# Kernel optimization log

Measured on AMD Instinct MI355X. Metric: run time of the kernel, lower is better.

The kernel has to match this reference:

```python
import jax, jax.numpy as jnp
import numpy as np
from jax import lax

DIM = 2048
N_HEADS = 16
N_KV = 4
HEAD_DIM = DIM // N_HEADS  # 128
ROPE_BASE = 10000.0
SEQ = 4096
BSZ = 1


def bitlinear(x, W):
    # per-row abs-mean scale (detached), ternary round/clamp, straight-through blend
    s = lax.stop_gradient(jnp.clip(jnp.mean(jnp.abs(W), axis=1, keepdims=True), 1e-5, None))
    wt = jnp.clip(jnp.round(W / s), -1.0, 1.0)
    w = lax.stop_gradient(wt - W) + W  # straight-through
    return x @ (w * s).T


def rms_norm(x):
    eps = jnp.finfo(x.dtype).eps
    return x * lax.rsqrt(jnp.mean(x * x, axis=-1, keepdims=True) + eps)


def rope(x, cos, sin):
    half = x.shape[-1] // 2
    x1, x2 = x[..., :half], x[..., half:]
    return jnp.concatenate((x1 * cos + x2 * sin, -x1 * sin + x2 * cos), axis=-1)


def setup_inputs() -> dict:
    key = jax.random.key(0)
    ks = jax.random.split(key, 6)
    kv_dim = N_KV * HEAD_DIM
    return {
        "x": jax.random.normal(ks[0], (BSZ, SEQ, DIM), dtype=jnp.float32),
        "wq": jax.random.normal(ks[1], (DIM, DIM), dtype=jnp.float32) * 0.02,
        "wk": jax.random.normal(ks[2], (kv_dim, DIM), dtype=jnp.float32) * 0.02,
        "wv": jax.random.normal(ks[3], (kv_dim, DIM), dtype=jnp.float32) * 0.02,
        "wp": jax.random.normal(ks[4], (DIM, DIM), dtype=jnp.float32) * 0.02,
        "q_gain": jnp.ones((N_HEADS,), dtype=jnp.float32),
    }


def reference(x, wq, wk, wv, wp, q_gain):
    b, s, d = x.shape
    q = bitlinear(x, wq).reshape(b, s, N_HEADS, HEAD_DIM).transpose(0, 2, 1, 3)  # bhsd
    k = bitlinear(x, wk).reshape(b, s, N_KV, HEAD_DIM).transpose(0, 2, 1, 3)
    v = bitlinear(x, wv).reshape(b, s, N_KV, HEAD_DIM).transpose(0, 2, 1, 3)

    q = rms_norm(q)
    k = rms_norm(k)

    inv_freq = 1.0 / ROPE_BASE ** (jnp.arange(0, HEAD_DIM, 2, dtype=jnp.float32) / HEAD_DIM)
    t = jnp.arange(s, dtype=jnp.float32)
    freqs = jnp.outer(t, inv_freq)  # [s, hd/2]
    cos = jnp.cos(freqs)[None, None].astype(q.dtype)
    sin = jnp.sin(freqs)[None, None].astype(q.dtype)
    q = rope(q, cos, sin)
    k = rope(k, cos, sin)

    q = q * q_gain.astype(q.dtype)[None, :, None, None]

    groups = N_HEADS // N_KV
    k = jnp.repeat(k, groups, axis=1)  # GQA expand to [b, H, s, hd]
    v = jnp.repeat(v, groups, axis=1)

    scale = 1.0 / np.sqrt(HEAD_DIM)
    scores = jnp.einsum("bhqd,bhkd->bhqk", q, k) * scale
    causal = jnp.tril(jnp.ones((s, s), dtype=bool))
    scores = jnp.where(causal[None, None], scores, jnp.finfo(scores.dtype).min)
    attn = jax.nn.softmax(scores, axis=-1)
    y = jnp.einsum("bhqk,bhkd->bhqd", attn, v)

    y = y.transpose(0, 2, 1, 3).reshape(b, s, d)
    return bitlinear(y, wp)
```

## Files before the change

### kernel.cpp

```cpp
#include <hip/hip_runtime.h>
#include <math.h>

typedef unsigned short u16;
typedef short s16x8 __attribute__((ext_vector_type(8)));
typedef short s16x4 __attribute__((ext_vector_type(4)));
typedef float f32x4 __attribute__((ext_vector_type(4)));
typedef u16 u16x4 __attribute__((ext_vector_type(4)));

static constexpr size_t OFF_XB   = 0;
static constexpr size_t OFF_WQKV = 16777216;
static constexpr size_t OFF_WP   = 29360128;
static constexpr size_t OFF_QKV  = 37748736;
static constexpr size_t OFF_Y    = 37748736 + 33554432;
static constexpr size_t OFF_KH   = 88080384;
static constexpr size_t OFF_VT   = 92274688;

__device__ __forceinline__ u16 f2bf(float f) {
  union { float f; unsigned u; } v; v.f = f;
  unsigned r = v.u + 0x7fffu + ((v.u >> 16) & 1u);
  return (u16)(r >> 16);
}

__device__ __forceinline__ float bf2f(u16 b) {
  union { unsigned u; float f; } v; v.u = ((unsigned)b) << 16;
  return v.f;
}

__device__ __forceinline__ void async16(const u16* g, u16* lds) {
  __builtin_amdgcn_global_load_lds(
      (const __attribute__((address_space(1))) void*)g,
      (__attribute__((address_space(3))) void*)lds, 16, 0, 0);
}

__global__ __launch_bounds__(256) void quant_rows(const float* __restrict__ W,
                                                  u16* __restrict__ out) {
  const int row = blockIdx.x, tid = threadIdx.x;
  const float* src = W + (size_t)row * 2048 + tid * 8;
  float4 a = *(const float4*)(src);
  float4 b = *(const float4*)(src + 4);
  float asum = fabsf(a.x)+fabsf(a.y)+fabsf(a.z)+fabsf(a.w)
             + fabsf(b.x)+fabsf(b.y)+fabsf(b.z)+fabsf(b.w);
  #pragma unroll
  for (int off = 1; off < 64; off <<= 1) asum += __shfl_xor(asum, off, 64);
  __shared__ float red[4];
  if ((tid & 63) == 0) red[tid >> 6] = asum;
  __syncthreads();
  float s = fmaxf((red[0]+red[1]+red[2]+red[3]) * (1.0f/2048.0f), 1e-5f);
  float v[8] = {a.x,a.y,a.z,a.w,b.x,b.y,b.z,b.w};
  u16* dst = out + (size_t)row * 2048 + tid * 8;
  #pragma unroll
  for (int i = 0; i < 8; i++) {
    float q = rintf(v[i] / s);
    q = fminf(fmaxf(q, -1.f), 1.f);
    dst[i] = f2bf(q * s);
  }
}

__global__ __launch_bounds__(256) void cvt_bf16(const float* __restrict__ in,
                                                u16* __restrict__ out) {
  size_t i = ((size_t)blockIdx.x * 256 + threadIdx.x) * 4;
  float4 v = *(const float4*)(in + i);
  u16x4 o;
  o.x = f2bf(v.x); o.y = f2bf(v.y); o.z = f2bf(v.z); o.w = f2bf(v.w);
  *(u16x4*)(out + i) = o;
}

__global__ __launch_bounds__(256) void gemm_bt(const u16* __restrict__ A,
                                               const u16* __restrict__ B,
                                               float* __restrict__ C,
                                               int M, int N, int K) {
  __shared__ u16 sA[128 * 32];
  __shared__ u16 sB[128 * 32];
  const int tid = threadIdx.x;
  const int lane = tid & 63;
  const int wid = tid >> 6;
  const int lr = lane & 15, lq = lane >> 4;
  const int wm = (wid >> 1) * 64, wn = (wid & 1) * 64;
  const size_t m0 = (size_t)blockIdx.y * 128, n0 = (size_t)blockIdx.x * 128;

  const int r0 = tid >> 2, c0 = (tid & 3) * 8;
  const u16* Ab0 = A + (m0 + r0) * (size_t)K + c0;
  const u16* Ab1 = A + (m0 + 64 + r0) * (size_t)K + c0;
  const u16* Bb0 = B + (n0 + r0) * (size_t)K + c0;
  const u16* Bb1 = B + (n0 + 64 + r0) * (size_t)K + c0;
  u16* sA0 = &sA[tid * 8];
  u16* sA1 = &sA[(256 + tid) * 8];
  u16* sB0 = &sB[tid * 8];
  u16* sB1 = &sB[(256 + tid) * 8];

  f32x4 acc[4][4] = {};

  for (int kt = 0; kt < K; kt += 32) {
    async16(Ab0 + kt, sA0);
    async16(Ab1 + kt, sA1);
    async16(Bb0 + kt, sB0);
    async16(Bb1 + kt, sB1);
    __syncthreads();
    s16x8 af[4], bf[4];
    #pragma unroll
    for (int mt = 0; mt < 4; mt++)
      af[mt] = *(const s16x8*)&sA[(wm + mt * 16 + lr) * 32 + lq * 8];
    #pragma unroll
    for (int nt = 0; nt < 4; nt++)
      bf[nt] = *(const s16x8*)&sB[(wn + nt * 16 + lr) * 32 + lq * 8];
    #pragma unroll
    for (int mt = 0; mt < 4; mt++)
      #pragma unroll
      for (int nt = 0; nt < 4; nt++)
        acc[mt][nt] = __builtin_amdgcn_mfma_f32_16x16x32_bf16(af[mt], bf[nt], acc[mt][nt], 0, 0, 0);
    __syncthreads();
  }
  #pragma unroll
  for (int mt = 0; mt < 4; mt++)
    #pragma unroll
    for (int nt = 0; nt < 4; nt++)
      #pragma unroll
      for (int r = 0; r < 4; r++) {
        size_t m = m0 + wm + mt * 16 + lq * 4 + r;
        size_t n = n0 + wn + nt * 16 + lr;
        C[m * (size_t)N + n] = acc[mt][nt][r];
      }
}

__global__ __launch_bounds__(256) void prep_qk(const float* __restrict__ qkv,
                                               const float* __restrict__ qgain,
                                               u16* __restrict__ Qh,
                                               u16* __restrict__ Kh) {
  const int s = blockIdx.y;
  const int j = blockIdx.x * 4 + (threadIdx.x >> 6);
  const int t = threadIdx.x & 63;
  const float* row = qkv + (size_t)s * 3072 + (size_t)j * 128;
  float x1 = row[t], x2 = row[t + 64];
  float ss = x1 * x1 + x2 * x2;
  #pragma unroll
  for (int off = 1; off < 64; off <<= 1) ss += __shfl_xor(ss, off, 64);
  float rn = rsqrtf(ss * (1.0f / 128.0f) + 1.1920929e-07f);
  float invf = exp2f(-(float)t * 0.20762050593048096f);
  float ang = (float)s * invf;
  float sn, c;
  sincosf(ang, &sn, &c);
  if (j < 16) {
    float g = qgain[j] * 0.12751738f;
    float q1 = x1 * rn, q2 = x2 * rn;
    float o1 = (q1 * c + q2 * sn) * g;
    float o2 = (-q1 * sn + q2 * c) * g;
    u16* dst = Qh + ((size_t)j * 4096 + s) * 128;
    dst[t] = f2bf(o1); dst[t + 64] = f2bf(o2);
  } else {
    float k1 = x1 * rn, k2 = x2 * rn;
    float o1 = k1 * c + k2 * sn;
    float o2 = -k1 * sn + k2 * c;
    u16* dst = Kh + ((size_t)(j - 16) * 4096 + s) * 128;
    dst[t] = f2bf(o1); dst[t + 64] = f2bf(o2);
  }
}

__global__ __launch_bounds__(256) void vtrans(const float* __restrict__ qkv,
                                              u16* __restrict__ Vtg) {
  __shared__ float tile[64][67];
  const int tid = threadIdx.x;
  const int s0 = blockIdx.y * 64;
  const int c0 = blockIdx.x * 64;
  #pragma unroll
  for (int it = 0; it < 4; it++) {
    int i = it * 256 + tid;
    int r = i >> 4, c = (i & 15) * 4;
    float4 v = *(const float4*)(qkv + (size_t)(s0 + r) * 3072 + 2560 + c0 + c);
    tile[r][c] = v.x; tile[r][c + 1] = v.y; tile[r][c + 2] = v.z; tile[r][c + 3] = v.w;
  }
  __syncthreads();
  #pragma unroll
  for (int it = 0; it < 2; it++) {
    int i = it * 256 + tid;
    int dl = i >> 3, sc = (i & 7) * 8;
    s16x8 ov;
    #pragma unroll
    for (int jj = 0; jj < 8; jj++) ov[jj] = (short)f2bf(tile[sc + jj][dl]);
    *(s16x8*)&Vtg[(size_t)(c0 + dl) * 4096 + s0 + sc] = ov;
  }
}

__global__ __launch_bounds__(256, 2) void attn(const u16* __restrict__ Q,
                                               const u16* __restrict__ Kh,
                                               const u16* __restrict__ Vt,
                                               u16* __restrict__ Opart,
                                               float* __restrict__ MLpart) {
  const int tid = threadIdx.x, lane = tid & 63, wid = tid >> 6;
  const int lr = lane & 15, lq = lane >> 4;

  const int b = blockIdx.x;
  const int h = b & 15;
  const int p = b >> 4;
  const int qt = 31 - (p >> 1);
  const int chunk = p & 1;
  const int t0 = chunk * (qt + 1);
  const int t1 = t0 + qt + 1;
  const int kvh = h >> 2;
  const int qbase = qt * 128;

  __shared__ u16 sK[64][136];
  __shared__ u16 sVt[128][72];

  s16x8 qf[2][4];
  #pragma unroll
  for (int f = 0; f < 2; f++) {
    const u16* qp = Q + ((size_t)h * 4096 + qbase + wid * 32 + f * 16 + lr) * 128 + lq * 8;
    #pragma unroll
    for (int kc = 0; kc < 4; kc++) qf[f][kc] = *(const s16x8*)(qp + kc * 32);
  }

  f32x4 oacc[2][8] = {};
  float mrow[2] = {-1e30f, -1e30f};
  float lrow[2] = {0.f, 0.f};

  const u16* Kbase = Kh + (size_t)kvh * 4096 * 128;
  const u16* Vbase = Vt + (size_t)kvh * 128 * 4096;

  for (int t = t0; t < t1; ++t) {
    #pragma unroll
    for (int it = 0; it < 4; it++) {
      int idx = it * 256 + tid;
      int kr = idx >> 4, kc8 = (idx & 15) * 8;
      *(s16x8*)&sK[kr][kc8] = *(const s16x8*)(Kbase + (size_t)(t * 64 + kr) * 128 + kc8);
    }
    #pragma unroll
    for (int it = 0; it < 4; it++) {
      int idx = it * 256 + tid;
      int vd = idx >> 3, vc = (idx & 7) * 8;
      s16x8 v = *(const s16x8*)(Vbase + (size_t)vd * 4096 + t * 64 + vc);
      int g0 = ((vc >> 2) & 3) * 16 + (vc >> 4) * 4;
      int g1 = (((vc >> 2) & 3) + 1) * 16 + (vc >> 4) * 4;
      s16x4 lo = {v[0], v[1], v[2], v[3]};
      s16x4 hi = {v[4], v[5], v[6], v[7]};
      *(s16x4*)&sVt[vd][g0] = lo;
      *(s16x4*)&sVt[vd][g1] = hi;
    }
    __syncthreads();

    f32x4 sacc[2][4] = {};
    #pragma unroll
    for (int nt = 0; nt < 4; nt++)
      #pragma unroll
      for (int kc = 0; kc < 4; kc++) {
        s16x8 kf = *(const s16x8*)&sK[nt * 16 + lr][kc * 32 + lq * 8];
        sacc[0][nt] = __builtin_amdgcn_mfma_f32_16x16x32_bf16(kf, qf[0][kc], sacc[0][nt], 0, 0, 0);
        sacc[1][nt] = __builtin_amdgcn_mfma_f32_16x16x32_bf16(kf, qf[1][kc], sacc[1][nt], 0, 0, 0);
      }

    if (t >= 2 * qt) {
      #pragma unroll
      for (int f = 0; f < 2; f++) {
        int qg = qbase + wid * 32 + f * 16 + lr;
        #pragma unroll
        for (int nt = 0; nt < 4; nt++) {
          int kv0 = t * 64 + nt * 16 + lq * 4;
          #pragma unroll
          for (int r = 0; r < 4; r++)
            if (kv0 + r > qg) sacc[f][nt][r] = -1e30f;
        }
      }
    }

    float mx[2];
    #pragma unroll
    for (int f = 0; f < 2; f++) {
      float m01 = fmaxf(fmaxf(sacc[f][0][0], sacc[f][0][1]), fmaxf(sacc[f][0][2], sacc[f][0][3]));
      float m23 = fmaxf(fmaxf(sacc[f][1][0], sacc[f][1][1]), fmaxf(sacc[f][1][2], sacc[f][1][3]));
      float m45 = fmaxf(fmaxf(sacc[f][2][0], sacc[f][2][1]), fmaxf(sacc[f][2][2], sacc[f][2][3]));
      float m67 = fmaxf(fmaxf(sacc[f][3][0], sacc[f][3][1]), fmaxf(sacc[f][3][2], sacc[f][3][3]));
      mx[f] = fmaxf(fmaxf(m01, m23), fmaxf(m45, m67));
      mx[f] = fmaxf(mx[f], __shfl_xor(mx[f], 16, 64));
      mx[f] = fmaxf(mx[f], __shfl_xor(mx[f], 32, 64));
    }

    bool grow = (mx[0] > mrow[0]) || (mx[1] > mrow[1]);
    if (__any(grow)) {
      #pragma unroll
      for (int f = 0; f < 2; f++) {
        float mn = fmaxf(mrow[f], mx[f]);
        float al = exp2f(mrow[f] - mn);
        mrow[f] = mn;
        lrow[f] *= al;
        #pragma unroll
        for (int dt = 0; dt < 8; dt++)
          #pragma unroll
          for (int r = 0; r < 4; r++) oacc[f][dt][r] *= al;
      }
    }

    s16x4 pf[2][4];
    float rsum[2] = {0.f, 0.f};
    #pragma unroll
    for (int f = 0; f < 2; f++)
      #pragma unroll
      for (int nt = 0; nt < 4; nt++)
        #pragma unroll
        for (int r = 0; r < 4; r++) {
          union { float fv; unsigned u; } pu;
          pu.fv = exp2f(sacc[f][nt][r] - mrow[f]);
          rsum[f] += pu.fv;
          pf[f][nt][r] = (short)(pu.u >> 16);
        }
    #pragma unroll
    for (int f = 0; f < 2; f++) {
      rsum[f] += __shfl_xor(rsum[f], 16, 64);
      rsum[f] += __shfl_xor(rsum[f], 32, 64);
      lrow[f] += rsum[f];
    }

    #pragma unroll
    for (int dt = 0; dt < 8; dt++) {
      s16x8 v01 = *(const s16x8*)&sVt[dt * 16 + lr][lq * 16];
      s16x8 v23 = *(const s16x8*)&sVt[dt * 16 + lr][lq * 16 + 8];
      s16x4 vf0 = {v01[0], v01[1], v01[2], v01[3]};
      s16x4 vf1 = {v01[4], v01[5], v01[6], v01[7]};
      s16x4 vf2 = {v23[0], v23[1], v23[2], v23[3]};
      s16x4 vf3 = {v23[4], v23[5], v23[6], v23[7]};
      #pragma unroll
      for (int f = 0; f < 2; f++) {
        oacc[f][dt] = __builtin_amdgcn_mfma_f32_16x16x16bf16_1k(vf0, pf[f][0], oacc[f][dt], 0, 0, 0);
        oacc[f][dt] = __builtin_amdgcn_mfma_f32_16x16x16bf16_1k(vf1, pf[f][1], oacc[f][dt], 0, 0, 0);
        oacc[f][dt] = __builtin_amdgcn_mfma_f32_16x16x16bf16_1k(vf2, pf[f][2], oacc[f][dt], 0, 0, 0);
        oacc[f][dt] = __builtin_amdgcn_mfma_f32_16x16x16bf16_1k(vf3, pf[f][3], oacc[f][dt], 0, 0, 0);
      }
    }
    __syncthreads();
  }

  u16* Op = Opart + (size_t)b * 16384;
  #pragma unroll
  for (int f = 0; f < 2; f++) {
    int row = wid * 32 + f * 16 + lr;
    #pragma unroll
    for (int dt = 0; dt < 8; dt++) {
      u16 tmp[4];
      #pragma unroll
      for (int r = 0; r < 4; r++) tmp[r] = f2bf(oacc[f][dt][r]);
      *(s16x4*)&Op[row * 128 + dt * 16 + lq * 4] = *(s16x4*)tmp;
    }
  }
  if (lq == 0) {
    #pragma unroll
    for (int f = 0; f < 2; f++) {
      int row = wid * 32 + f * 16 + lr;
      MLpart[(size_t)b * 256 + row * 2]     = mrow[f];
      MLpart[(size_t)b * 256 + row * 2 + 1] = lrow[f];
    }
  }
}

__global__ __launch_bounds__(256) void combine(const u16* __restrict__ Op,
                                               const float* __restrict__ ML,
                                               u16* __restrict__ Y) {
  const int blk = blockIdx.x;
  const int qtc = blk >> 4, h = blk & 15;
  const int qt = 31 - qtc;
  const int b0 = (qtc * 2) * 16 + h, b1 = b0 + 16;
  const int tid = threadIdx.x;
  const int row = tid >> 1, half = (tid & 1) * 64;
  float m0 = ML[(size_t)b0 * 256 + row * 2], l0 = ML[(size_t)b0 * 256 + row * 2 + 1];
  float m1 = ML[(size_t)b1 * 256 + row * 2], l1 = ML[(size_t)b1 * 256 + row * 2 + 1];
  float m = fmaxf(m0, m1);
  float w0 = exp2f(m0 - m), w1 = exp2f(m1 - m);
  float inv = 1.0f / (l0 * w0 + l1 * w1);
  w0 *= inv; w1 *= inv;
  const u16* o0 = Op + (size_t)b0 * 16384 + row * 128 + half;
  const u16* o1 = Op + (size_t)b1 * 16384 + row * 128 + half;
  size_t q = (size_t)qt * 128 + row;
  u16* dst = Y + q * 2048 + h * 128 + half;
  #pragma unroll
  for (int c = 0; c < 64; c += 8) {
    s16x8 a0 = *(const s16x8*)(o0 + c);
    s16x8 a1 = *(const s16x8*)(o1 + c);
    u16 tmp[8];
    #pragma unroll
    for (int jj = 0; jj < 8; jj++)
      tmp[jj] = f2bf(bf2f((u16)a0[jj]) * w0 + bf2f((u16)a1[jj]) * w1);
    *(s16x8*)(dst + c) = *(s16x8*)tmp;
  }
}

extern "C" void kernel_launch(void* const* d_in, const int* in_sizes, int n_in,
                              void* d_out, int out_size, void* d_ws, size_t ws_size,
                              hipStream_t stream) {
  const float* x  = (const float*)d_in[0];
  const float* wq = (const float*)d_in[1];
  const float* wk = (const float*)d_in[2];
  const float* wv = (const float*)d_in[3];
  const float* wp = (const float*)d_in[4];
  const float* qg = (const float*)d_in[5];
  float* out = (float*)d_out;
  char* ws = (char*)d_ws;

  u16*   XB    = (u16*)(ws + OFF_XB);
  u16*   WQKV  = (u16*)(ws + OFF_WQKV);
  u16*   WP    = (u16*)(ws + OFF_WP);
  float* QKV   = (float*)(ws + OFF_QKV);
  u16*   QH    = XB;
  u16*   KH    = (u16*)(ws + OFF_KH);
  u16*   VT    = (u16*)(ws + OFF_VT);
  u16*   OPART = (u16*)(ws + OFF_QKV);
  u16*   Yb    = (u16*)(ws + OFF_Y);
  float* MLP   = (float*)(ws + OFF_WQKV);

  quant_rows<<<2048, 256, 0, stream>>>(wq, WQKV);
  quant_rows<<<512,  256, 0, stream>>>(wk, WQKV + (size_t)2048 * 2048);
  quant_rows<<<512,  256, 0, stream>>>(wv, WQKV + (size_t)2560 * 2048);
  quant_rows<<<2048, 256, 0, stream>>>(wp, WP);
  cvt_bf16<<<8192, 256, 0, stream>>>(x, XB);
  gemm_bt<<<dim3(24, 32), 256, 0, stream>>>(XB, WQKV, QKV, 4096, 3072, 2048);
  prep_qk<<<dim3(5, 4096), 256, 0, stream>>>(QKV, qg, QH, KH);
  vtrans<<<dim3(8, 64), 256, 0, stream>>>(QKV, VT);
  attn<<<1024, 256, 0, stream>>>(QH, KH, VT, OPART, MLP);
  combine<<<512, 256, 0, stream>>>(OPART, MLP, Yb);
  gemm_bt<<<dim3(16, 32), 256, 0, stream>>>(Yb, WP, out, 4096, 2048, 2048);
}
```

Measured before the change: 419.9 us.

## Balance causal attention work with a precomputed segment table and direct writes

New measurement: 418.1 us. Within noise of the previous version (-0.4%).

```diff
diff --git a/kernel.cpp b/kernel.cpp
--- a/kernel.cpp
+++ b/kernel.cpp
@@ -9,11 +9,12 @@
 
 static constexpr size_t OFF_XB   = 0;
 static constexpr size_t OFF_WQKV = 16777216;
+static constexpr size_t OFF_KH   = 16777216;
+static constexpr size_t OFF_VT   = 20971520;
+static constexpr size_t OFF_ML   = 25165824;
 static constexpr size_t OFF_WP   = 29360128;
 static constexpr size_t OFF_QKV  = 37748736;
-static constexpr size_t OFF_Y    = 37748736 + 33554432;
-static constexpr size_t OFF_KH   = 88080384;
-static constexpr size_t OFF_VT   = 92274688;
+static constexpr size_t OFF_Y    = 79691776;
 
 __device__ __forceinline__ u16 f2bf(float f) {
   union { float f; unsigned u; } v; v.f = f;
@@ -180,171 +181,258 @@
   }
 }
 
+#define SEG(qt,a,b,s) ((unsigned)((qt)|((a)<<5)|((b)<<11)|((s)<<18)))
+__constant__ unsigned SEGTAB[128] = {
+  SEG(0,0,2,127),   SEG(15,0,15,14),
+  SEG(15,15,32,15), 0,
+  SEG(1,0,4,127),   SEG(14,0,13,12),
+  SEG(14,13,30,13), 0,
+  SEG(2,0,6,127),   SEG(13,0,11,10),
+  SEG(13,11,28,11), 0,
+  SEG(3,0,8,127),   SEG(12,0,9,8),
+  SEG(12,9,26,9),   0,
+  SEG(4,0,10,127),  SEG(11,0,7,6),
+  SEG(11,7,24,7),   0,
+  SEG(5,0,12,127),  SEG(10,0,5,4),
+  SEG(10,5,22,5),   0,
+  SEG(6,0,14,127),  SEG(9,0,3,2),
+  SEG(9,3,20,3),    0,
+  SEG(7,0,16,127),  SEG(8,0,1,0),
+  SEG(8,1,18,1),    0,
+  SEG(16,0,16,16),  0,
+  SEG(16,16,33,17), 0,
+  SEG(16,33,34,18), SEG(17,0,15,19),
+  SEG(17,15,31,20), 0,
+  SEG(17,31,36,21), SEG(18,0,12,22),
+  SEG(18,12,28,23), 0,
+  SEG(18,28,38,24), SEG(19,0,6,25),
+  SEG(19,6,23,26),  0,
+  SEG(19,23,39,27), 0,
+  SEG(19,39,40,28), SEG(20,0,15,29),
+  SEG(20,15,32,30), 0,
+  SEG(20,32,42,31), SEG(21,0,6,32),
+  SEG(21,6,22,33),  0,
+  SEG(21,22,39,34), 0,
+  SEG(21,39,44,35), SEG(22,0,11,36),
+  SEG(22,11,27,37), 0,
+  SEG(22,27,44,38), 0,
+  SEG(22,44,46,39), SEG(23,0,14,40),
+  SEG(23,14,30,41), 0,
+  SEG(23,30,47,42), 0,
+  SEG(23,47,48,43), SEG(24,0,15,44),
+  SEG(24,15,31,45), 0,
+  SEG(24,31,48,46), 0,
+  SEG(24,48,50,47), SEG(25,0,14,48),
+  SEG(25,14,30,49), 0,
+  SEG(25,30,47,50), 0,
+  SEG(25,47,52,51), SEG(26,0,11,52),
+  SEG(26,11,27,53), 0,
+  SEG(26,27,44,54), 0,
+  SEG(26,44,54,55), SEG(27,0,6,56),
+  SEG(27,6,22,57),  0,
+  SEG(27,22,39,58), 0,
+  SEG(27,39,55,59), 0,
+  SEG(27,55,56,60), SEG(28,0,15,61),
+  SEG(28,15,32,62), 0,
+  SEG(28,32,48,63), 0,
+  SEG(28,48,58,64), SEG(29,0,6,65),
+  SEG(29,6,23,66),  0,
+  SEG(29,23,39,67), 0,
+  SEG(29,39,55,68), 0,
+  SEG(29,55,60,69), SEG(30,0,12,70),
+  SEG(30,12,28,71), 0,
+  SEG(30,28,44,72), 0,
+  SEG(30,44,61,73), 0,
+  SEG(30,61,62,74), SEG(31,0,15,75),
+  SEG(31,15,31,76), 0,
+  SEG(31,31,48,77), 0,
+  SEG(31,48,64,78), 0,
+};
+__constant__ unsigned char CBASE[24] = {0,2,4,6,8,10,12,14, 16,19,22,25,29,32,36,40, 44,48,52,56,61,65,70,75};
+__constant__ unsigned char CCNT[24]  = {2,2,2,2,2,2,2,2, 3,3,3,4,3,4,4,4, 4,4,4,5,4,5,5,4};
+
 __global__ __launch_bounds__(256, 2) void attn(const u16* __restrict__ Q,
                                                const u16* __restrict__ Kh,
                                                const u16* __restrict__ Vt,
+                                               u16* __restrict__ Y,
                                                u16* __restrict__ Opart,
                                                float* __restrict__ MLpart) {
   const int tid = threadIdx.x, lane = tid & 63, wid = tid >> 6;
   const int lr = lane & 15, lq = lane >> 4;
-
   const int b = blockIdx.x;
-  const int h = b & 15;
-  const int p = b >> 4;
-  const int qt = 31 - (p >> 1);
-  const int chunk = p & 1;
-  const int t0 = chunk * (qt + 1);
-  const int t1 = t0 + qt + 1;
+  const int h = b & 15, unit = b >> 4;
   const int kvh = h >> 2;
-  const int qbase = qt * 128;
 
   __shared__ u16 sK[64][136];
   __shared__ u16 sVt[128][72];
 
-  s16x8 qf[2][4];
-  #pragma unroll
-  for (int f = 0; f < 2; f++) {
-    const u16* qp = Q + ((size_t)h * 4096 + qbase + wid * 32 + f * 16 + lr) * 128 + lq * 8;
-    #pragma unroll
-    for (int kc = 0; kc < 4; kc++) qf[f][kc] = *(const s16x8*)(qp + kc * 32);
-  }
-
-  f32x4 oacc[2][8] = {};
-  float mrow[2] = {-1e30f, -1e30f};
-  float lrow[2] = {0.f, 0.f};
-
   const u16* Kbase = Kh + (size_t)kvh * 4096 * 128;
   const u16* Vbase = Vt + (size_t)kvh * 128 * 4096;
 
-  for (int t = t0; t < t1; ++t) {
-    #pragma unroll
-    for (int it = 0; it < 4; it++) {
-      int idx = it * 256 + tid;
-      int kr = idx >> 4, kc8 = (idx & 15) * 8;
-      *(s16x8*)&sK[kr][kc8] = *(const s16x8*)(Kbase + (size_t)(t * 64 + kr) * 128 + kc8);
+  #pragma unroll 1
+  for (int si = 0; si < 2; ++si) {
+    const unsigned sd = SEGTAB[unit * 2 + si];
+    const int qt = sd & 31;
+    const int t0 = (sd >> 5) & 63;
+    const int t1 = (sd >> 11) & 127;
+    const int slot = (sd >> 18) & 127;
+    if (t1 <= t0) continue;
+    const int qbase = qt * 128;
+
+    s16x8 qf[2][4];
+    #pragma unroll
+    for (int f = 0; f < 2; f++) {
+      const u16* qp = Q + ((size_t)h * 4096 + qbase + wid * 32 + f * 16 + lr) * 128 + lq * 8;
+      #pragma unroll
+      for (int kc = 0; kc < 4; kc++) qf[f][kc] = *(const s16x8*)(qp + kc * 32);
     }
-    #pragma unroll
-    for (int it = 0; it < 4; it++) {
-      int idx = it * 256 + tid;
-      int vd = idx >> 3, vc = (idx & 7) * 8;
-      s16x8 v = *(const s16x8*)(Vbase + (size_t)vd * 4096 + t * 64 + vc);
-      int g0 = ((vc >> 2) & 3) * 16 + (vc >> 4) * 4;
-      int g1 = (((vc >> 2) & 3) + 1) * 16 + (vc >> 4) * 4;
-      s16x4 lo = {v[0], v[1], v[2], v[3]};
-      s16x4 hi = {v[4], v[5], v[6], v[7]};
-      *(s16x4*)&sVt[vd][g0] = lo;
-      *(s16x4*)&sVt[vd][g1] = hi;
+
+    f32x4 oacc[2][8] = {};
+    float mrow[2] = {-1e30f, -1e30f};
+    float lrow[2] = {0.f, 0.f};
+
+    for (int t = t0; t < t1; ++t) {
+      #pragma unroll
+      for (int it = 0; it < 4; it++) {
+        int idx = it * 256 + tid;
+        int kr = idx >> 4, kc8 = (idx & 15) * 8;
+        *(s16x8*)&sK[kr][kc8] = *(const s16x8*)(Kbase + (size_t)(t * 64 + kr) * 128 + kc8);
+      }
+      #pragma unroll
+      for (int it = 0; it < 4; it++) {
+        int idx = it * 256 + tid;
+        int vd = idx >> 3, vc = (idx & 7) * 8;
+        s16x8 v = *(const s16x8*)(Vbase + (size_t)vd * 4096 + t * 64 + vc);
+        int g0 = ((vc >> 2) & 3) * 16 + (vc >> 4) * 4;
+        int g1 = (((vc >> 2) & 3) + 1) * 16 + (vc >> 4) * 4;
+        s16x4 lo = {v[0], v[1], v[2], v[3]};
+        s16x4 hi = {v[4], v[5], v[6], v[7]};
+        *(s16x4*)&sVt[vd][g0] = lo;
+        *(s16x4*)&sVt[vd][g1] = hi;
+      }
+      __syncthreads();
+
+      f32x4 sacc[2][4] = {};
+      #pragma unroll
+      for (int nt = 0; nt < 4; nt++)
+        #pragma unroll
+        for (int kc = 0; kc < 4; kc++) {
+          s16x8 kf = *(const s16x8*)&sK[nt * 16 + lr][kc * 32 + lq * 8];
+          sacc[0][nt] = __builtin_amdgcn_mfma_f32_16x16x32_bf16(kf, qf[0][kc], sacc[0][nt], 0, 0, 0);
+          sacc[1][nt] = __builtin_amdgcn_mfma_f32_16x16x32_bf16(kf, qf[1][kc], sacc[1][nt], 0, 0, 0);
+        }
+
+      if (t >= 2 * qt) {
+        #pragma unroll
+        for (int f = 0; f < 2; f++) {
+          int qg = qbase + wid * 32 + f * 16 + lr;
+          #pragma unroll
+          for (int nt = 0; nt < 4; nt++) {
+            int kv0 = t * 64 + nt * 16 + lq * 4;
+            #pragma unroll
+            for (int r = 0; r < 4; r++)
+              if (kv0 + r > qg) sacc[f][nt][r] = -1e30f;
+          }
+        }
+      }
+
+      float mx[2];
+      #pragma unroll
+      for (int f = 0; f < 2; f++) {
+        float m01 = fmaxf(fmaxf(sacc[f][0][0], sacc[f][0][1]), fmaxf(sacc[f][0][2], sacc[f][0][3]));
+        float m23 = fmaxf(fmaxf(sacc[f][1][0], sacc[f][1][1]), fmaxf(sacc[f][1][2], sacc[f][1][3]));
+        float m45 = fmaxf(fmaxf(sacc[f][2][0], sacc[f][2][1]), fmaxf(sacc[f][2][2], sacc[f][2][3]));
+        float m67 = fmaxf(fmaxf(sacc[f][3][0], sacc[f][3][1]), fmaxf(sacc[f][3][2], sacc[f][3][3]));
+        mx[f] = fmaxf(fmaxf(m01, m23), fmaxf(m45, m67));
+        mx[f] = fmaxf(mx[f], __shfl_xor(mx[f], 16, 64));
+        mx[f] = fmaxf(mx[f], __shfl_xor(mx[f], 32, 64));
+      }
+
+      bool grow = (mx[0] > mrow[0]) || (mx[1] > mrow[1]);
+      if (__any(grow)) {
+        #pragma unroll
+        for (int f = 0; f < 2; f++) {
+          float mn = fmaxf(mrow[f], mx[f]);
+          float al = exp2f(mrow[f] - mn);
+          mrow[f] = mn;
+          lrow[f] *= al;
+          #pragma unroll
+          for (int dt = 0; dt < 8; dt++)
+            #pragma unroll
+            for (int r = 0; r < 4; r++) oacc[f][dt][r] *= al;
+        }
+      }
+
+      s16x4 pf[2][4];
+      float rsum[2] = {0.f, 0.f};
+      #pragma unroll
+      for (int f = 0; f < 2; f++)
+        #pragma unroll
+        for (int nt = 0; nt < 4; nt++)
+          #pragma unroll
+          for (int r = 0; r < 4; r++) {
+            union { float fv; unsigned u; } pu;
+            pu.fv = exp2f(sacc[f][nt][r] - mrow[f]);
+            rsum[f] += pu.fv;
+            pf[f][nt][r] = (short)(pu.u >> 16);
+          }
+      #pragma unroll
+      for (int f = 0; f < 2; f++) {
+        rsum[f] += __shfl_xor(rsum[f], 16, 64);
+        rsum[f] += __shfl_xor(rsum[f], 32, 64);
+        lrow[f] += rsum[f];
+      }
+
+      #pragma unroll
+      for (int dt = 0; dt < 8; dt++) {
+        s16x8 v01 = *(const s16x8*)&sVt[dt * 16 + lr][lq * 16];
+        s16x8 v23 = *(const s16x8*)&sVt[dt * 16 + lr][lq * 16 + 8];
+        s16x4 vf0 = {v01[0], v01[1], v01[2], v01[3]};
+        s16x4 vf1 = {v01[4], v01[5], v01[6], v01[7]};
+        s16x4 vf2 = {v23[0], v23[1], v23[2], v23[3]};
+        s16x4 vf3 = {v23[4], v23[5], v23[6], v23[7]};
+        #pragma unroll
+        for (int f = 0; f < 2; f++) {
+          oacc[f][dt] = __builtin_amdgcn_mfma_f32_16x16x16bf16_1k(vf0, pf[f][0], oacc[f][dt], 0, 0, 0);
+          oacc[f][dt] = __builtin_amdgcn_mfma_f32_16x16x16bf16_1k(vf1, pf[f][1], oacc[f][dt], 0, 0, 0);
+          oacc[f][dt] = __builtin_amdgcn_mfma_f32_16x16x16bf16_1k(vf2, pf[f][2], oacc[f][dt], 0, 0, 0);
+          oacc[f][dt] = __builtin_amdgcn_mfma_f32_16x16x16bf16_1k(vf3, pf[f][3], oacc[f][dt], 0, 0, 0);
+        }
+      }
+      __syncthreads();
     }
-    __syncthreads();
-
-    f32x4 sacc[2][4] = {};
-    #pragma unroll
-    for (int nt = 0; nt < 4; nt++)
-      #pragma unroll
-      for (int kc = 0; kc < 4; kc++) {
-        s16x8 kf = *(const s16x8*)&sK[nt * 16 + lr][kc * 32 + lq * 8];
-        sacc[0][nt] = __builtin_amdgcn_mfma_f32_16x16x32_bf16(kf, qf[0][kc], sacc[0][nt], 0, 0, 0);
-        sacc[1][nt] = __builtin_amdgcn_mfma_f32_16x16x32_bf16(kf, qf[1][kc], sacc[1][nt], 0, 0, 0);
-      }
-
-    if (t >= 2 * qt) {
+
+    if (slot == 127) {
       #pragma unroll
       for (int f = 0; f < 2; f++) {
+        float linv = 1.0f / lrow[f];
         int qg = qbase + wid * 32 + f * 16 + lr;
         #pragma unroll
-        for (int nt = 0; nt < 4; nt++) {
-          int kv0 = t * 64 + nt * 16 + lq * 4;
+        for (int dt = 0; dt < 8; dt++) {
+          u16 tmp[4];
           #pragma unroll
-          for (int r = 0; r < 4; r++)
-            if (kv0 + r > qg) sacc[f][nt][r] = -1e30f;
-        }
-      }
-    }
-
-    float mx[2];
-    #pragma unroll
-    for (int f = 0; f < 2; f++) {
-      float m01 = fmaxf(fmaxf(sacc[f][0][0], sacc[f][0][1]), fmaxf(sacc[f][0][2], sacc[f][0][3]));
-      float m23 = fmaxf(fmaxf(sacc[f][1][0], sacc[f][1][1]), fmaxf(sacc[f][1][2], sacc[f][1][3]));
-      float m45 = fmaxf(fmaxf(sacc[f][2][0], sacc[f][2][1]), fmaxf(sacc[f][2][2], sacc[f][2][3]));
-      float m67 = fmaxf(fmaxf(sacc[f][3][0], sacc[f][3][1]), fmaxf(sacc[f][3][2], sacc[f][3][3]));
-      mx[f] = fmaxf(fmaxf(m01, m23), fmaxf(m45, m67));
-      mx[f] = fmaxf(mx[f], __shfl_xor(mx[f], 16, 64));
-      mx[f] = fmaxf(mx[f], __shfl_xor(mx[f], 32, 64));
-    }
-
-    bool grow = (mx[0] > mrow[0]) || (mx[1] > mrow[1]);
-    if (__any(grow)) {
+          for (int r = 0; r < 4; r++) tmp[r] = f2bf(oacc[f][dt][r] * linv);
+          *(s16x4*)&Y[(size_t)qg * 2048 + h * 128 + dt * 16 + lq * 4] = *(s16x4*)tmp;
+        }
+      }
+    } else {
+      const int gslot = h * 79 + slot;
+      u16* Op = Opart + (size_t)gslot * 16384;
       #pragma unroll
       for (int f = 0; f < 2; f++) {
-        float mn = fmaxf(mrow[f], mx[f]);
-        float al = exp2f(mrow[f] - mn);
-        mrow[f] = mn;
-        lrow[f] *= al;
-        #pragma unroll
-        for (int dt = 0; dt < 8; dt++)
+        int row = wid * 32 + f * 16 + lr;
+        #pragma unroll
+        for (int dt = 0; dt < 8; dt++) {
+          u16 tmp[4];
           #pragma unroll
-          for (int r = 0; r < 4; r++) oacc[f][dt][r] *= al;
-      }
-    }
-
-    s16x4 pf[2][4];
-    float rsum[2] = {0.f, 0.f};
-    #pragma unroll
-    for (int f = 0; f < 2; f++)
-      #pragma unroll
-      for (int nt = 0; nt < 4; nt++)
-        #pragma unroll
-        for (int r = 0; r < 4; r++) {
-          union { float fv; unsigned u; } pu;
-          pu.fv = exp2f(sacc[f][nt][r] - mrow[f]);
-          rsum[f] += pu.fv;
-          pf[f][nt][r] = (short)(pu.u >> 16);
-        }
-    #pragma unroll
-    for (int f = 0; f < 2; f++) {
-      rsum[f] += __shfl_xor(rsum[f], 16, 64);
-      rsum[f] += __shfl_xor(rsum[f], 32, 64);
-      lrow[f] += rsum[f];
-    }
-
-    #pragma unroll
-    for (int dt = 0; dt < 8; dt++) {
-      s16x8 v01 = *(const s16x8*)&sVt[dt * 16 + lr][lq * 16];
-      s16x8 v23 = *(const s16x8*)&sVt[dt * 16 + lr][lq * 16 + 8];
-      s16x4 vf0 = {v01[0], v01[1], v01[2], v01[3]};
-      s16x4 vf1 = {v01[4], v01[5], v01[6], v01[7]};
-      s16x4 vf2 = {v23[0], v23[1], v23[2], v23[3]};
-      s16x4 vf3 = {v23[4], v23[5], v23[6], v23[7]};
-      #pragma unroll
-      for (int f = 0; f < 2; f++) {
-        oacc[f][dt] = __builtin_amdgcn_mfma_f32_16x16x16bf16_1k(vf0, pf[f][0], oacc[f][dt], 0, 0, 0);
-        oacc[f][dt] = __builtin_amdgcn_mfma_f32_16x16x16bf16_1k(vf1, pf[f][1], oacc[f][dt], 0, 0, 0);
-        oacc[f][dt] = __builtin_amdgcn_mfma_f32_16x16x16bf16_1k(vf2, pf[f][2], oacc[f][dt], 0, 0, 0);
-        oacc[f][dt] = __builtin_amdgcn_mfma_f32_16x16x16bf16_1k(vf3, pf[f][3], oacc[f][dt], 0, 0, 0);
-      }
-    }
-    __syncthreads();
-  }
-
-  u16* Op = Opart + (size_t)b * 16384;
-  #pragma unroll
-  for (int f = 0; f < 2; f++) {
-    int row = wid * 32 + f * 16 + lr;
-    #pragma unroll
-    for (int dt = 0; dt < 8; dt++) {
-      u16 tmp[4];
-      #pragma unroll
-      for (int r = 0; r < 4; r++) tmp[r] = f2bf(oacc[f][dt][r]);
-      *(s16x4*)&Op[row * 128 + dt * 16 + lq * 4] = *(s16x4*)tmp;
-    }
-  }
-  if (lq == 0) {
-    #pragma unroll
-    for (int f = 0; f < 2; f++) {
-      int row = wid * 32 + f * 16 + lr;
-      MLpart[(size_t)b * 256 + row * 2]     = mrow[f];
-      MLpart[(size_t)b * 256 + row * 2 + 1] = lrow[f];
+          for (int r = 0; r < 4; r++) tmp[r] = f2bf(oacc[f][dt][r]);
+          *(s16x4*)&Op[row * 128 + dt * 16 + lq * 4] = *(s16x4*)tmp;
+        }
+        if (lq == 0) {
+          MLpart[(size_t)gslot * 256 + row * 2]     = mrow[f];
+          MLpart[(size_t)gslot * 256 + row * 2 + 1] = lrow[f];
+        }
+      }
     }
   }
 }
@@ -352,30 +440,41 @@
 __global__ __launch_bounds__(256) void combine(const u16* __restrict__ Op,
                                                const float* __restrict__ ML,
                                                u16* __restrict__ Y) {
-  const int blk = blockIdx.x;
-  const int qtc = blk >> 4, h = blk & 15;
-  const int qt = 31 - qtc;
-  const int b0 = (qtc * 2) * 16 + h, b1 = b0 + 16;
+  const int b = blockIdx.x;
+  const int qt = 8 + (b >> 4), h = b & 15;
+  const int base = CBASE[qt - 8], n = CCNT[qt - 8];
+  const int gbase = h * 79 + base;
   const int tid = threadIdx.x;
   const int row = tid >> 1, half = (tid & 1) * 64;
-  float m0 = ML[(size_t)b0 * 256 + row * 2], l0 = ML[(size_t)b0 * 256 + row * 2 + 1];
-  float m1 = ML[(size_t)b1 * 256 + row * 2], l1 = ML[(size_t)b1 * 256 + row * 2 + 1];
-  float m = fmaxf(m0, m1);
-  float w0 = exp2f(m0 - m), w1 = exp2f(m1 - m);
-  float inv = 1.0f / (l0 * w0 + l1 * w1);
-  w0 *= inv; w1 *= inv;
-  const u16* o0 = Op + (size_t)b0 * 16384 + row * 128 + half;
-  const u16* o1 = Op + (size_t)b1 * 16384 + row * 128 + half;
-  size_t q = (size_t)qt * 128 + row;
-  u16* dst = Y + q * 2048 + h * 128 + half;
+
+  float m[5], l[5];
+  float mstar = -3e38f;
+  for (int i = 0; i < n; i++) {
+    m[i] = ML[(size_t)(gbase + i) * 256 + row * 2];
+    l[i] = ML[(size_t)(gbase + i) * 256 + row * 2 + 1];
+    mstar = fmaxf(mstar, m[i]);
+  }
+  float w[5], wsum = 0.f;
+  for (int i = 0; i < n; i++) { w[i] = exp2f(m[i] - mstar); wsum += l[i] * w[i]; }
+  float inv = 1.0f / wsum;
+
+  float acc[64] = {};
+  for (int i = 0; i < n; i++) {
+    const u16* o = Op + (size_t)(gbase + i) * 16384 + row * 128 + half;
+    float wi = w[i];
+    #pragma unroll
+    for (int c = 0; c < 64; c += 8) {
+      s16x8 a = *(const s16x8*)(o + c);
+      #pragma unroll
+      for (int jj = 0; jj < 8; jj++) acc[c + jj] += wi * bf2f((u16)a[jj]);
+    }
+  }
+  u16* dst = Y + ((size_t)qt * 128 + row) * 2048 + h * 128 + half;
   #pragma unroll
   for (int c = 0; c < 64; c += 8) {
-    s16x8 a0 = *(const s16x8*)(o0 + c);
-    s16x8 a1 = *(const s16x8*)(o1 + c);
     u16 tmp[8];
     #pragma unroll
-    for (int jj = 0; jj < 8; jj++)
-      tmp[jj] = f2bf(bf2f((u16)a0[jj]) * w0 + bf2f((u16)a1[jj]) * w1);
+    for (int jj = 0; jj < 8; jj++) tmp[jj] = f2bf(acc[c + jj] * inv);
     *(s16x8*)(dst + c) = *(s16x8*)tmp;
   }
 }
@@ -399,9 +498,9 @@
   u16*   QH    = XB;
   u16*   KH    = (u16*)(ws + OFF_KH);
   u16*   VT    = (u16*)(ws + OFF_VT);
+  float* MLP   = (float*)(ws + OFF_ML);
   u16*   OPART = (u16*)(ws + OFF_QKV);
   u16*   Yb    = (u16*)(ws + OFF_Y);
-  float* MLP   = (float*)(ws + OFF_WQKV);
 
   quant_rows<<<2048, 256, 0, stream>>>(wq, WQKV);
   quant_rows<<<512,  256, 0, stream>>>(wk, WQKV + (size_t)2048 * 2048);
@@ -411,7 +510,7 @@
   gemm_bt<<<dim3(24, 32), 256, 0, stream>>>(XB, WQKV, QKV, 4096, 3072, 2048);
   prep_qk<<<dim3(5, 4096), 256, 0, stream>>>(QKV, qg, QH, KH);
   vtrans<<<dim3(8, 64), 256, 0, stream>>>(QKV, VT);
-  attn<<<1024, 256, 0, stream>>>(QH, KH, VT, OPART, MLP);
-  combine<<<512, 256, 0, stream>>>(OPART, MLP, Yb);
+  attn<<<1024, 256, 0, stream>>>(QH, KH, VT, Yb, OPART, MLP);
+  combine<<<384, 256, 0, stream>>>(OPART, MLP, Yb);
   gemm_bt<<<dim3(16, 32), 256, 0, stream>>>(Yb, WP, out, 4096, 2048, 2048);
 }
```
